# Kernel optimization log

Measured on AMD Instinct MI355X. Metric: run time of the kernel, lower is better.

The kernel has to match this reference:

```python
import jax, jax.numpy as jnp
import numpy as np

LATENT = 256
OUT_CH = 1
K = 16
HEADS = 64


def _conv1x1(x, W, b):
    # x: [B, Cin, ...spatial], W: [Cout, Cin], b: [Cout]
    y = jnp.einsum('oc,bc...->bo...', W, x)
    return y + b.reshape((1, -1) + (1,) * (y.ndim - 2))


def _batch_gather(x, idx):
    # x: [B, C, N], idx: [B, Nq, K] -> [B, C, Nq, K]
    return jax.vmap(lambda xb, ib: xb[:, ib])(x, idx)


def setup_inputs() -> dict:
    key = jax.random.key(0)
    ks = jax.random.split(key, 16)
    B, N, NQ = 2, 10000, 10000
    inp = {
        'latents': jax.random.normal(ks[0], (B, LATENT, N), jnp.float32),
        'pts': jax.random.normal(ks[1], (B, 3, N), jnp.float32),
        'pts_query': jax.random.normal(ks[2], (B, 3, NQ), jnp.float32),
        'proj_ids': jax.random.randint(ks[3], (B, NQ, K), 0, N, jnp.int64),
    }
    def lin(k, o, i):
        s = 1.0 / np.sqrt(i)
        k1, k2 = jax.random.split(k)
        return (jax.random.uniform(k1, (o, i), jnp.float32, -s, s),
                jax.random.uniform(k2, (o,), jnp.float32, -s, s))
    inp['W1'], inp['b1'] = lin(ks[4], LATENT, LATENT + 3)
    inp['W2'], inp['b2'] = lin(ks[5], LATENT, LATENT)
    inp['W3'], inp['b3'] = lin(ks[6], LATENT, LATENT)
    inp['Wq'], inp['bq'] = lin(ks[7], HEADS, LATENT)
    inp['Wv'], inp['bv'] = lin(ks[8], LATENT, LATENT)
    inp['W8'], inp['b8'] = lin(ks[9], OUT_CH, LATENT)
    return inp


def reference(latents, pts, pts_query, proj_ids,
              W1, b1, W2, b2, W3, b3, Wq, bq, Wv, bv, W8, b8):
    # gather neighbor latents and points: [B, C, Nq, K], [B, 3, Nq, K]
    x = _batch_gather(latents, proj_ids)
    npts = _batch_gather(pts, proj_ids)
    rel = pts_query[:, :, :, None] - npts          # [B, 3, Nq, K]
    x = jnp.concatenate([x, rel], axis=1)          # [B, C+3, Nq, K]
    x = jax.nn.relu(_conv1x1(x, W1, b1))
    x = jax.nn.relu(_conv1x1(x, W2, b2))
    x = jax.nn.relu(_conv1x1(x, W3, b3))
    query = _conv1x1(x, Wq, bq)                    # [B, 64, Nq, K]
    value = _conv1x1(x, Wv, bv)                    # [B, C, Nq, K]
    attention = jax.nn.softmax(query, axis=-1).mean(axis=1)  # [B, Nq, K]
    # weighted sum over K neighbors: [B, Nq, C] -> [B, C, Nq]
    x = jnp.einsum('bnk,bcnk->bcn', attention, value)
    x = _conv1x1(x, W8, b8)                        # [B, out_ch, Nq]
    return x
```

## Files before the change

kernel.cpp:

```cpp
#include <hip/hip_runtime.h>
#include <cstdint>
#include <cstddef>


#define NLAT 256
#define KNB 16
#define QB 4
#define MROWS 64
#define ROWB 560

typedef float    f32x4  __attribute__((ext_vector_type(4)));
typedef float    f32x16 __attribute__((ext_vector_type(16)));
typedef _Float16 f16x8  __attribute__((ext_vector_type(8)));
typedef _Float16 f16x4  __attribute__((ext_vector_type(4)));

struct Smem {
  unsigned char buf[MROWS * ROWB];
  float Sp[4][MROWS];
  float Sv[MROWS];
  int sidx[MROWS];
  int is64;
};

__device__ __forceinline__ void layer_mfma32(
    unsigned char* __restrict__ buf, const unsigned short* __restrict__ Wp,
    const float* __restrict__ bias, const float* __restrict__ W1f,
    int lane, int wave, bool relu)
{
  const int lm32 = lane & 31, h = lane >> 5;
  const char* bp = (const char*)buf + lm32 * 560 + h * 16;
  const char* wbase = (const char*)Wp + (wave * 2) * 1024 + lm32 * 32 + h * 16;

  f32x16 acc[2][2];
#pragma unroll
  for (int i = 0; i < 2; ++i)
#pragma unroll
    for (int j = 0; j < 2; ++j) acc[i][j] = (f32x16)(0.f);

#pragma unroll
  for (int ks = 0; ks < 16; ++ks) {
    f16x8 a[2], b[2];
#pragma unroll
    for (int ct = 0; ct < 2; ++ct)
      a[ct] = *(const f16x8*)(wbase + ks * 8192 + ct * 1024);
#pragma unroll
    for (int mt = 0; mt < 2; ++mt)
      b[mt] = *(const f16x8*)(bp + mt * 17920 + ks * 32);
#pragma unroll
    for (int ct = 0; ct < 2; ++ct)
#pragma unroll
      for (int mt = 0; mt < 2; ++mt)
        acc[ct][mt] = __builtin_amdgcn_mfma_f32_32x32x16_f16(a[ct], b[mt], acc[ct][mt], 0, 0, 0);
  }
  if (W1f) {
    f16x8 a[2], b[2];
#pragma unroll
    for (int ct = 0; ct < 2; ++ct) {
      f16x8 v = {0, 0, 0, 0, 0, 0, 0, 0};
      if (h == 0) {
        const int ch = (wave * 2 + ct) * 32 + lm32;
        const float* wt = W1f + (size_t)ch * 259 + 256;
        v[0] = (_Float16)wt[0]; v[1] = (_Float16)wt[1]; v[2] = (_Float16)wt[2];
      }
      a[ct] = v;
    }
#pragma unroll
    for (int mt = 0; mt < 2; ++mt)
      b[mt] = *(const f16x8*)(bp + mt * 17920 + 512);
#pragma unroll
    for (int ct = 0; ct < 2; ++ct)
#pragma unroll
      for (int mt = 0; mt < 2; ++mt)
        acc[ct][mt] = __builtin_amdgcn_mfma_f32_32x32x16_f16(a[ct], b[mt], acc[ct][mt], 0, 0, 0);
  }
  __syncthreads();
#pragma unroll
  for (int ct = 0; ct < 2; ++ct) {
#pragma unroll
    for (int q = 0; q < 4; ++q) {
      const int ch0 = (wave * 2 + ct) * 32 + q * 8 + h * 4;
      const float4 bs = *(const float4*)(bias + ch0);
      const float bb[4] = {bs.x, bs.y, bs.z, bs.w};
#pragma unroll
      for (int mt = 0; mt < 2; ++mt) {
        f16x4 v;
#pragma unroll
        for (int j = 0; j < 4; ++j) {
          float x = acc[ct][mt][q * 4 + j] + bb[j];
          if (relu) x = fmaxf(x, 0.f);
          v[j] = (_Float16)x;
        }
        *(f16x4*)((char*)buf + (mt * 32 + lm32) * 560 + ch0 * 2) = v;
      }
    }
  }
}

extern "C" __global__ __launch_bounds__(256, 4)
void interp_mfma(const float* __restrict__ latents,
                 const float* __restrict__ pts,
                 const float* __restrict__ ptsq,
                 const void*  __restrict__ proj,
                 const unsigned short* __restrict__ Lt_u,
                 const float* __restrict__ W1f,
                 const unsigned short* __restrict__ W1p,
                 const unsigned short* __restrict__ W2p,
                 const unsigned short* __restrict__ W3p,
                 const unsigned short* __restrict__ Wqh,
                 const float* __restrict__ b1, const float* __restrict__ b2,
                 const float* __restrict__ b3, const float* __restrict__ bq,
                 const float* __restrict__ wv8, const float* __restrict__ c0p,
                 float* __restrict__ out,
                 int N, int NQ, int use_lt)
{
  __shared__ Smem sm;
  const int tid = threadIdx.x;
  const int bid = blockIdx.x;
  const int lane = tid & 63, wave = tid >> 6;
  const int lm = lane & 15, lk = lane >> 4;

  if (tid == 0) {
    const int* p = (const int*)proj;
    int z = 1;
    for (int i = 0; i < 64; ++i) z &= (p[2 * i + 1] == 0);
    sm.is64 = z;
  }
  __syncthreads();
  if (tid < MROWS) {
    long long g = (long long)bid * QB + (tid >> 4);
    long long base = g * KNB + (tid & 15);
    sm.sidx[tid] = sm.is64 ? (int)((const long long*)proj)[base]
                           : ((const int*)proj)[base];
  }
  __syncthreads();

  {
    const int row = tid & 63, part = tid >> 6;
    const int id = sm.sidx[row];
    const long long g = (long long)bid * QB + (row >> 4);
    const int b = (int)(g / NQ);
    char* dst = (char*)sm.buf + row * 560 + part * 128;
    if (use_lt) {
      const _Float16* src = (const _Float16*)Lt_u + ((size_t)b * N + id) * NLAT + part * 64;
#pragma unroll
      for (int cc = 0; cc < 8; ++cc)
        *(f16x8*)(dst + cc * 16) = *(const f16x8*)(src + cc * 8);
    } else {
      for (int cc = 0; cc < 8; ++cc) {
        f16x8 v;
#pragma unroll
        for (int e = 0; e < 8; ++e)
          v[e] = (_Float16)latents[((size_t)b * NLAT + part * 64 + cc * 8 + e) * N + id];
        *(f16x8*)(dst + cc * 16) = v;
      }
    }
    if (part == 0) {
      const int nq = (int)(g - (long long)b * NQ);
      f16x8 v = {0, 0, 0, 0, 0, 0, 0, 0};
#pragma unroll
      for (int j = 0; j < 3; ++j)
        v[j] = (_Float16)(ptsq[((size_t)b * 3 + j) * NQ + nq]
                        - pts[((size_t)b * 3 + j) * N + id]);
      const f16x8 z = {0, 0, 0, 0, 0, 0, 0, 0};
      *(f16x8*)((char*)sm.buf + row * 560 + 512) = v;
      *(f16x8*)((char*)sm.buf + row * 560 + 528) = z;
    }
  }
  __syncthreads();

  layer_mfma32(sm.buf, W1p, b1, W1f, lane, wave, true);
  __syncthreads();
  layer_mfma32(sm.buf, W2p, b2, nullptr, lane, wave, true);
  __syncthreads();
  layer_mfma32(sm.buf, W3p, b3, nullptr, lane, wave, true);
  __syncthreads();

  const char* bp16 = (const char*)sm.buf + lm * 560 + lk * 16;
  f32x4 qacc[4];
#pragma unroll
  for (int mt = 0; mt < 4; ++mt) qacc[mt] = (f32x4){0.f, 0.f, 0.f, 0.f};
  {
    const char* wqb = (const char*)Wqh + (wave * 16 + lm) * 512 + lk * 16;
#pragma unroll
    for (int ks = 0; ks < 8; ++ks) {
      f16x8 a = *(const f16x8*)(wqb + ks * 64);
#pragma unroll
      for (int mt = 0; mt < 4; ++mt) {
        f16x8 bf = *(const f16x8*)(bp16 + mt * 8960 + ks * 64);
        qacc[mt] = __builtin_amdgcn_mfma_f32_16x16x32_f16(a, bf, qacc[mt], 0, 0, 0);
      }
    }
  }
  {
    const char* sp = (const char*)sm.buf + (wave * 16 + lm) * 560 + lk * 16;
    float sacc = 0.f;
#pragma unroll
    for (int cc = 0; cc < 8; ++cc) {
      f16x8 v = *(const f16x8*)(sp + cc * 64);
      const int k0 = cc * 32 + lk * 8;
      const float4 w0 = *(const float4*)(wv8 + k0);
      const float4 w1 = *(const float4*)(wv8 + k0 + 4);
      sacc += (float)v[0] * w0.x + (float)v[1] * w0.y
            + (float)v[2] * w0.z + (float)v[3] * w0.w;
      sacc += (float)v[4] * w1.x + (float)v[5] * w1.y
            + (float)v[6] * w1.z + (float)v[7] * w1.w;
    }
    sacc += __shfl_xor(sacc, 16);
    sacc += __shfl_xor(sacc, 32);
    if (lk == 0) sm.Sv[wave * 16 + lm] = sacc;
  }

  {
    float bqv[4];
#pragma unroll
    for (int r = 0; r < 4; ++r) bqv[r] = bq[wave * 16 + lk * 4 + r];
#pragma unroll
    for (int mt = 0; mt < 4; ++mt) {
      float sw = 0.f;
#pragma unroll
      for (int r = 0; r < 4; ++r) {
        const float qv = qacc[mt][r] + bqv[r];
        float mx = qv;
#pragma unroll
        for (int msk = 1; msk < 16; msk <<= 1) mx = fmaxf(mx, __shfl_xor(mx, msk));
        const float e = __expf(qv - mx);
        float s = e;
#pragma unroll
        for (int msk = 1; msk < 16; msk <<= 1) s += __shfl_xor(s, msk);
        sw += e / s;
      }
      sw += __shfl_xor(sw, 16);
      sw += __shfl_xor(sw, 32);
      if (lk == 0) sm.Sp[wave][mt * 16 + lm] = sw;
    }
  }
  __syncthreads();

  {
    const int m = wave * 16 + lm;
    const float a = (sm.Sp[0][m] + sm.Sp[1][m] + sm.Sp[2][m] + sm.Sp[3][m]) * (1.f / 64.f);
    float val = a * sm.Sv[m];
#pragma unroll
    for (int msk = 1; msk < 16; msk <<= 1) val += __shfl_xor(val, msk);
    if (lane == 0) out[(long long)bid * QB + wave] = val + c0p[0];
  }
}

extern "C" __global__ void prep_w(const float* __restrict__ W1, const float* __restrict__ W2,
                                  const float* __restrict__ W3, const float* __restrict__ Wq,
                                  const float* __restrict__ Wv, const float* __restrict__ W8,
                                  const float* __restrict__ bv, const float* __restrict__ b8,
                                  unsigned short* W1p, unsigned short* W2p,
                                  unsigned short* W3p, unsigned short* Wqh,
                                  float* wv8, float* c0) {
  const int t = blockIdx.x * 256 + threadIdx.x;
  union { _Float16 h; unsigned short u; } cv;
  if (t < 65536) {
    const int ch = t >> 8, k = t & 255;
    const int dst = (k >> 4) * 4096 + ch * 16 + ((k >> 3) & 1) * 8 + (k & 7);
    cv.h = (_Float16)W1[(size_t)ch * 259 + k]; W1p[dst] = cv.u;
    cv.h = (_Float16)W2[t]; W2p[dst] = cv.u;
    cv.h = (_Float16)W3[t]; W3p[dst] = cv.u;
  }
  if (t < 16384) { cv.h = (_Float16)Wq[t]; Wqh[t] = cv.u; }
  if (t < 256) {
    float s = 0.f;
    for (int o = 0; o < 256; ++o) s += Wv[(size_t)o * 256 + t] * W8[o];
    wv8[t] = s;
  }
  if (t == 0) {
    float s = 0.f;
    for (int o = 0; o < 256; ++o) s += bv[o] * W8[o];
    c0[0] = s + b8[0];
  }
}

extern "C" __global__ void transp(const float* __restrict__ latents,
                                  unsigned short* __restrict__ Lt, int N) {
  __shared__ unsigned short tile[256][68];
  const int b = blockIdx.y, n0 = blockIdx.x * 64, tid = threadIdx.x;
  const int nl = tid & 63;
  union { _Float16 h; unsigned short u; } cv;
  for (int c = tid >> 6; c < 256; c += 4) {
    const int n = n0 + nl;
    float v = (n < N) ? latents[((size_t)b * NLAT + c) * N + n] : 0.f;
    cv.h = (_Float16)v;
    tile[c][nl] = cv.u;
  }
  __syncthreads();
  const int nr = tid >> 2, cg = (tid & 3) * 64;
  const int n = n0 + nr;
  if (n < N) {
    for (int cc = 0; cc < 64; cc += 8) {
      f16x8 v;
#pragma unroll
      for (int j = 0; j < 8; ++j) {
        union { unsigned short u; _Float16 h; } bk;
        bk.u = tile[cg + cc + j][nr];
        v[j] = bk.h;
      }
      *(f16x8*)((_Float16*)Lt + ((size_t)b * N + n) * NLAT + cg + cc) = v;
    }
  }
}

extern "C" void kernel_launch(void* const* d_in, const int* in_sizes, int n_in,
                              void* d_out, int out_size, void* d_ws, size_t ws_size,
                              hipStream_t stream) {
  (void)n_in; (void)out_size;
  const float* latents = (const float*)d_in[0];
  const float* pts     = (const float*)d_in[1];
  const float* ptsq    = (const float*)d_in[2];
  const void*  proj    = d_in[3];
  const float* W1 = (const float*)d_in[4];  const float* b1 = (const float*)d_in[5];
  const float* W2 = (const float*)d_in[6];  const float* b2 = (const float*)d_in[7];
  const float* W3 = (const float*)d_in[8];  const float* b3 = (const float*)d_in[9];
  const float* Wq = (const float*)d_in[10]; const float* bq = (const float*)d_in[11];
  const float* Wv = (const float*)d_in[12]; const float* bv = (const float*)d_in[13];
  const float* W8 = (const float*)d_in[14]; const float* b8 = (const float*)d_in[15];
  float* out = (float*)d_out;

  const int B  = 2;
  const int N  = in_sizes[1] / (3 * B);
  const int NQ = in_sizes[2] / (3 * B);

  size_t off = 0;
  auto alloc = [&](size_t bytes) -> char* {
    char* p = (char*)d_ws + off;
    off += (bytes + 255) & ~(size_t)255;
    return p;
  };
  unsigned short* W1p = (unsigned short*)alloc(65536 * 2);
  unsigned short* W2p = (unsigned short*)alloc(65536 * 2);
  unsigned short* W3p = (unsigned short*)alloc(65536 * 2);
  unsigned short* Wqh = (unsigned short*)alloc(16384 * 2);
  float* wv8 = (float*)alloc(256 * 4);
  float* c0  = (float*)alloc(4);
  const size_t lt_bytes = (size_t)B * N * NLAT * 2;
  unsigned short* Lt = (unsigned short*)((char*)d_ws + off);
  const int use_lt = (off + lt_bytes <= ws_size) ? 1 : 0;

  hipLaunchKernelGGL(prep_w, dim3(256), dim3(256), 0, stream,
                     W1, W2, W3, Wq, Wv, W8, bv, b8, W1p, W2p, W3p, Wqh, wv8, c0);
  if (use_lt)
    hipLaunchKernelGGL(transp, dim3((N + 63) / 64, B), dim3(256), 0, stream,
                       latents, Lt, N);
  const int nblocks = (B * NQ + QB - 1) / QB;
  hipLaunchKernelGGL(interp_mfma, dim3(nblocks), dim3(256), 0, stream,
                     latents, pts, ptsq, proj, Lt, W1, W1p, W2p, W3p, Wqh,
                     b1, b2, b3, bq, wv8, c0, out, N, NQ, use_lt);
}
```

Measured before the change: 219.5 us.

## Double rows per block and give each wave full query heads locally

```diff
diff --git a/kernel.cpp b/kernel.cpp
--- a/kernel.cpp
+++ b/kernel.cpp
@@ -5,22 +5,14 @@
 
 #define NLAT 256
 #define KNB 16
-#define QB 4
-#define MROWS 64
+#define QB 8
+#define MROWS 128
 #define ROWB 560
 
 typedef float    f32x4  __attribute__((ext_vector_type(4)));
 typedef float    f32x16 __attribute__((ext_vector_type(16)));
 typedef _Float16 f16x8  __attribute__((ext_vector_type(8)));
 typedef _Float16 f16x4  __attribute__((ext_vector_type(4)));
-
-struct Smem {
-  unsigned char buf[MROWS * ROWB];
-  float Sp[4][MROWS];
-  float Sv[MROWS];
-  int sidx[MROWS];
-  int is64;
-};
 
 __device__ __forceinline__ void layer_mfma32(
     unsigned char* __restrict__ buf, const unsigned short* __restrict__ Wp,
@@ -29,48 +21,48 @@
 {
   const int lm32 = lane & 31, h = lane >> 5;
   const char* bp = (const char*)buf + lm32 * 560 + h * 16;
-  const char* wbase = (const char*)Wp + (wave * 2) * 1024 + lm32 * 32 + h * 16;
-
-  f32x16 acc[2][2];
+  const char* wbase = (const char*)Wp + (wave * 64 + lm32) * 32 + h * 16;
+
+  f32x16 acc[2][4];
 #pragma unroll
   for (int i = 0; i < 2; ++i)
 #pragma unroll
-    for (int j = 0; j < 2; ++j) acc[i][j] = (f32x16)(0.f);
+    for (int j = 0; j < 4; ++j) acc[i][j] = (f32x16)(0.f);
 
 #pragma unroll
   for (int ks = 0; ks < 16; ++ks) {
-    f16x8 a[2], b[2];
+    f16x8 a[2], b[4];
 #pragma unroll
     for (int ct = 0; ct < 2; ++ct)
       a[ct] = *(const f16x8*)(wbase + ks * 8192 + ct * 1024);
 #pragma unroll
-    for (int mt = 0; mt < 2; ++mt)
+    for (int mt = 0; mt < 4; ++mt)
       b[mt] = *(const f16x8*)(bp + mt * 17920 + ks * 32);
 #pragma unroll
     for (int ct = 0; ct < 2; ++ct)
 #pragma unroll
-      for (int mt = 0; mt < 2; ++mt)
+      for (int mt = 0; mt < 4; ++mt)
         acc[ct][mt] = __builtin_amdgcn_mfma_f32_32x32x16_f16(a[ct], b[mt], acc[ct][mt], 0, 0, 0);
   }
   if (W1f) {
-    f16x8 a[2], b[2];
+    f16x8 a[2], b[4];
 #pragma unroll
     for (int ct = 0; ct < 2; ++ct) {
       f16x8 v = {0, 0, 0, 0, 0, 0, 0, 0};
       if (h == 0) {
-        const int ch = (wave * 2 + ct) * 32 + lm32;
+        const int ch = wave * 64 + ct * 32 + lm32;
         const float* wt = W1f + (size_t)ch * 259 + 256;
         v[0] = (_Float16)wt[0]; v[1] = (_Float16)wt[1]; v[2] = (_Float16)wt[2];
       }
       a[ct] = v;
     }
 #pragma unroll
-    for (int mt = 0; mt < 2; ++mt)
+    for (int mt = 0; mt < 4; ++mt)
       b[mt] = *(const f16x8*)(bp + mt * 17920 + 512);
 #pragma unroll
     for (int ct = 0; ct < 2; ++ct)
 #pragma unroll
-      for (int mt = 0; mt < 2; ++mt)
+      for (int mt = 0; mt < 4; ++mt)
         acc[ct][mt] = __builtin_amdgcn_mfma_f32_32x32x16_f16(a[ct], b[mt], acc[ct][mt], 0, 0, 0);
   }
   __syncthreads();
@@ -78,11 +70,11 @@
   for (int ct = 0; ct < 2; ++ct) {
 #pragma unroll
     for (int q = 0; q < 4; ++q) {
-      const int ch0 = (wave * 2 + ct) * 32 + q * 8 + h * 4;
+      const int ch0 = wave * 64 + ct * 32 + q * 8 + h * 4;
       const float4 bs = *(const float4*)(bias + ch0);
       const float bb[4] = {bs.x, bs.y, bs.z, bs.w};
 #pragma unroll
-      for (int mt = 0; mt < 2; ++mt) {
+      for (int mt = 0; mt < 4; ++mt) {
         f16x4 v;
 #pragma unroll
         for (int j = 0; j < 4; ++j) {
@@ -96,7 +88,7 @@
   }
 }
 
-extern "C" __global__ __launch_bounds__(256, 4)
+extern "C" __global__ __launch_bounds__(256, 2)
 void interp_mfma(const float* __restrict__ latents,
                  const float* __restrict__ pts,
                  const float* __restrict__ ptsq,
@@ -113,44 +105,39 @@
                  float* __restrict__ out,
                  int N, int NQ, int use_lt)
 {
-  __shared__ Smem sm;
+  __shared__ unsigned char buf[MROWS * ROWB];
   const int tid = threadIdx.x;
   const int bid = blockIdx.x;
   const int lane = tid & 63, wave = tid >> 6;
   const int lm = lane & 15, lk = lane >> 4;
 
-  if (tid == 0) {
+  int is64;
+  {
     const int* p = (const int*)proj;
     int z = 1;
     for (int i = 0; i < 64; ++i) z &= (p[2 * i + 1] == 0);
-    sm.is64 = z;
-  }
-  __syncthreads();
-  if (tid < MROWS) {
-    long long g = (long long)bid * QB + (tid >> 4);
-    long long base = g * KNB + (tid & 15);
-    sm.sidx[tid] = sm.is64 ? (int)((const long long*)proj)[base]
-                           : ((const int*)proj)[base];
-  }
-  __syncthreads();
+    is64 = z;
+  }
 
   {
-    const int row = tid & 63, part = tid >> 6;
-    const int id = sm.sidx[row];
+    const int row = tid & 127, part = tid >> 7;
     const long long g = (long long)bid * QB + (row >> 4);
+    const long long pbase = g * KNB + (row & 15);
+    const int id = is64 ? (int)((const long long*)proj)[pbase]
+                        : ((const int*)proj)[pbase];
     const int b = (int)(g / NQ);
-    char* dst = (char*)sm.buf + row * 560 + part * 128;
+    char* dst = (char*)buf + row * 560 + part * 256;
     if (use_lt) {
-      const _Float16* src = (const _Float16*)Lt_u + ((size_t)b * N + id) * NLAT + part * 64;
-#pragma unroll
-      for (int cc = 0; cc < 8; ++cc)
+      const _Float16* src = (const _Float16*)Lt_u + ((size_t)b * N + id) * NLAT + part * 128;
+#pragma unroll
+      for (int cc = 0; cc < 16; ++cc)
         *(f16x8*)(dst + cc * 16) = *(const f16x8*)(src + cc * 8);
     } else {
-      for (int cc = 0; cc < 8; ++cc) {
+      for (int cc = 0; cc < 16; ++cc) {
         f16x8 v;
 #pragma unroll
         for (int e = 0; e < 8; ++e)
-          v[e] = (_Float16)latents[((size_t)b * NLAT + part * 64 + cc * 8 + e) * N + id];
+          v[e] = (_Float16)latents[((size_t)b * NLAT + part * 128 + cc * 8 + e) * N + id];
         *(f16x8*)(dst + cc * 16) = v;
       }
     }
@@ -162,37 +149,47 @@
         v[j] = (_Float16)(ptsq[((size_t)b * 3 + j) * NQ + nq]
                         - pts[((size_t)b * 3 + j) * N + id]);
       const f16x8 z = {0, 0, 0, 0, 0, 0, 0, 0};
-      *(f16x8*)((char*)sm.buf + row * 560 + 512) = v;
-      *(f16x8*)((char*)sm.buf + row * 560 + 528) = z;
-    }
-  }
-  __syncthreads();
-
-  layer_mfma32(sm.buf, W1p, b1, W1f, lane, wave, true);
-  __syncthreads();
-  layer_mfma32(sm.buf, W2p, b2, nullptr, lane, wave, true);
-  __syncthreads();
-  layer_mfma32(sm.buf, W3p, b3, nullptr, lane, wave, true);
-  __syncthreads();
-
-  const char* bp16 = (const char*)sm.buf + lm * 560 + lk * 16;
-  f32x4 qacc[4];
-#pragma unroll
-  for (int mt = 0; mt < 4; ++mt) qacc[mt] = (f32x4){0.f, 0.f, 0.f, 0.f};
+      *(f16x8*)((char*)buf + row * 560 + 512) = v;
+      *(f16x8*)((char*)buf + row * 560 + 528) = z;
+    }
+  }
+  __syncthreads();
+
+  layer_mfma32(buf, W1p, b1, W1f, lane, wave, true);
+  __syncthreads();
+  layer_mfma32(buf, W2p, b2, nullptr, lane, wave, true);
+  __syncthreads();
+  layer_mfma32(buf, W3p, b3, nullptr, lane, wave, true);
+  __syncthreads();
+
+  const char* bp16 = (const char*)buf + (wave * 32 + lm) * 560 + lk * 16;
+  f32x4 qacc[4][2];
+#pragma unroll
+  for (int ht = 0; ht < 4; ++ht)
+#pragma unroll
+    for (int mt = 0; mt < 2; ++mt) qacc[ht][mt] = (f32x4){0.f, 0.f, 0.f, 0.f};
   {
-    const char* wqb = (const char*)Wqh + (wave * 16 + lm) * 512 + lk * 16;
 #pragma unroll
     for (int ks = 0; ks < 8; ++ks) {
-      f16x8 a = *(const f16x8*)(wqb + ks * 64);
-#pragma unroll
-      for (int mt = 0; mt < 4; ++mt) {
-        f16x8 bf = *(const f16x8*)(bp16 + mt * 8960 + ks * 64);
-        qacc[mt] = __builtin_amdgcn_mfma_f32_16x16x32_f16(a, bf, qacc[mt], 0, 0, 0);
-      }
-    }
-  }
-  {
-    const char* sp = (const char*)sm.buf + (wave * 16 + lm) * 560 + lk * 16;
+      f16x8 a[4], b[2];
+#pragma unroll
+      for (int ht = 0; ht < 4; ++ht)
+        a[ht] = *(const f16x8*)((const char*)Wqh + (ht * 16 + lm) * 512 + ks * 64 + lk * 16);
+#pragma unroll
+      for (int mt = 0; mt < 2; ++mt)
+        b[mt] = *(const f16x8*)(bp16 + mt * 8960 + ks * 64);
+#pragma unroll
+      for (int ht = 0; ht < 4; ++ht)
+#pragma unroll
+        for (int mt = 0; mt < 2; ++mt)
+          qacc[ht][mt] = __builtin_amdgcn_mfma_f32_16x16x32_f16(a[ht], b[mt], qacc[ht][mt], 0, 0, 0);
+    }
+  }
+
+  float sv[2];
+#pragma unroll
+  for (int sg = 0; sg < 2; ++sg) {
+    const char* sp = (const char*)buf + (wave * 32 + sg * 16 + lm) * 560 + lk * 16;
     float sacc = 0.f;
 #pragma unroll
     for (int cc = 0; cc < 8; ++cc) {
@@ -207,42 +204,41 @@
     }
     sacc += __shfl_xor(sacc, 16);
     sacc += __shfl_xor(sacc, 32);
-    if (lk == 0) sm.Sv[wave * 16 + lm] = sacc;
+    sv[sg] = sacc;
   }
 
   {
-    float bqv[4];
-#pragma unroll
-    for (int r = 0; r < 4; ++r) bqv[r] = bq[wave * 16 + lk * 4 + r];
-#pragma unroll
-    for (int mt = 0; mt < 4; ++mt) {
+    float bqv[4][4];
+#pragma unroll
+    for (int ht = 0; ht < 4; ++ht) {
+      const float4 bv4 = *(const float4*)(bq + ht * 16 + lk * 4);
+      bqv[ht][0] = bv4.x; bqv[ht][1] = bv4.y; bqv[ht][2] = bv4.z; bqv[ht][3] = bv4.w;
+    }
+#pragma unroll
+    for (int sg = 0; sg < 2; ++sg) {
       float sw = 0.f;
 #pragma unroll
-      for (int r = 0; r < 4; ++r) {
-        const float qv = qacc[mt][r] + bqv[r];
-        float mx = qv;
-#pragma unroll
-        for (int msk = 1; msk < 16; msk <<= 1) mx = fmaxf(mx, __shfl_xor(mx, msk));
-        const float e = __expf(qv - mx);
-        float s = e;
-#pragma unroll
-        for (int msk = 1; msk < 16; msk <<= 1) s += __shfl_xor(s, msk);
-        sw += e / s;
+      for (int ht = 0; ht < 4; ++ht) {
+#pragma unroll
+        for (int r = 0; r < 4; ++r) {
+          const float qv = qacc[ht][sg][r] + bqv[ht][r];
+          float mx = qv;
+#pragma unroll
+          for (int msk = 1; msk < 16; msk <<= 1) mx = fmaxf(mx, __shfl_xor(mx, msk));
+          const float e = __expf(qv - mx);
+          float s = e;
+#pragma unroll
+          for (int msk = 1; msk < 16; msk <<= 1) s += __shfl_xor(s, msk);
+          sw += e / s;
+        }
       }
       sw += __shfl_xor(sw, 16);
       sw += __shfl_xor(sw, 32);
-      if (lk == 0) sm.Sp[wave][mt * 16 + lm] = sw;
-    }
-  }
-  __syncthreads();
-
-  {
-    const int m = wave * 16 + lm;
-    const float a = (sm.Sp[0][m] + sm.Sp[1][m] + sm.Sp[2][m] + sm.Sp[3][m]) * (1.f / 64.f);
-    float val = a * sm.Sv[m];
-#pragma unroll
-    for (int msk = 1; msk < 16; msk <<= 1) val += __shfl_xor(val, msk);
-    if (lane == 0) out[(long long)bid * QB + wave] = val + c0p[0];
+      float val = sw * (1.f / 64.f) * sv[sg];
+#pragma unroll
+      for (int msk = 1; msk < 16; msk <<= 1) val += __shfl_xor(val, msk);
+      if (lane == 0) out[(long long)bid * QB + wave * 2 + sg] = val + c0p[0];
+    }
   }
 }
 
```

Result: slower. 248.8 us (+13.4%).

## Precompute layer-1 projection per source point before gathering neighbors

Applied to the files above, without the earlier changes.

```diff
diff --git a/kernel.cpp b/kernel.cpp
--- a/kernel.cpp
+++ b/kernel.cpp
@@ -7,7 +7,8 @@
 #define KNB 16
 #define QB 4
 #define MROWS 64
-#define ROWB 560
+#define ROWB 528
+#define MTSTR 16896
 
 typedef float    f32x4  __attribute__((ext_vector_type(4)));
 typedef float    f32x16 __attribute__((ext_vector_type(16)));
@@ -24,12 +25,11 @@
 
 __device__ __forceinline__ void layer_mfma32(
     unsigned char* __restrict__ buf, const unsigned short* __restrict__ Wp,
-    const float* __restrict__ bias, const float* __restrict__ W1f,
-    int lane, int wave, bool relu)
+    const float* __restrict__ bias, int lane, int wave, bool relu)
 {
   const int lm32 = lane & 31, h = lane >> 5;
-  const char* bp = (const char*)buf + lm32 * 560 + h * 16;
-  const char* wbase = (const char*)Wp + (wave * 2) * 1024 + lm32 * 32 + h * 16;
+  const char* bp = (const char*)buf + lm32 * 528 + h * 16;
+  const char* wbase = (const char*)Wp + (wave * 64 + lm32) * 32 + h * 16;
 
   f32x16 acc[2][2];
 #pragma unroll
@@ -45,40 +45,19 @@
       a[ct] = *(const f16x8*)(wbase + ks * 8192 + ct * 1024);
 #pragma unroll
     for (int mt = 0; mt < 2; ++mt)
-      b[mt] = *(const f16x8*)(bp + mt * 17920 + ks * 32);
+      b[mt] = *(const f16x8*)(bp + mt * MTSTR + ks * 32);
 #pragma unroll
     for (int ct = 0; ct < 2; ++ct)
 #pragma unroll
       for (int mt = 0; mt < 2; ++mt)
         acc[ct][mt] = __builtin_amdgcn_mfma_f32_32x32x16_f16(a[ct], b[mt], acc[ct][mt], 0, 0, 0);
   }
-  if (W1f) {
-    f16x8 a[2], b[2];
-#pragma unroll
-    for (int ct = 0; ct < 2; ++ct) {
-      f16x8 v = {0, 0, 0, 0, 0, 0, 0, 0};
-      if (h == 0) {
-        const int ch = (wave * 2 + ct) * 32 + lm32;
-        const float* wt = W1f + (size_t)ch * 259 + 256;
-        v[0] = (_Float16)wt[0]; v[1] = (_Float16)wt[1]; v[2] = (_Float16)wt[2];
-      }
-      a[ct] = v;
-    }
-#pragma unroll
-    for (int mt = 0; mt < 2; ++mt)
-      b[mt] = *(const f16x8*)(bp + mt * 17920 + 512);
-#pragma unroll
-    for (int ct = 0; ct < 2; ++ct)
-#pragma unroll
-      for (int mt = 0; mt < 2; ++mt)
-        acc[ct][mt] = __builtin_amdgcn_mfma_f32_32x32x16_f16(a[ct], b[mt], acc[ct][mt], 0, 0, 0);
-  }
   __syncthreads();
 #pragma unroll
   for (int ct = 0; ct < 2; ++ct) {
 #pragma unroll
     for (int q = 0; q < 4; ++q) {
-      const int ch0 = (wave * 2 + ct) * 32 + q * 8 + h * 4;
+      const int ch0 = wave * 64 + ct * 32 + q * 8 + h * 4;
       const float4 bs = *(const float4*)(bias + ch0);
       const float bb[4] = {bs.x, bs.y, bs.z, bs.w};
 #pragma unroll
@@ -90,28 +69,26 @@
           if (relu) x = fmaxf(x, 0.f);
           v[j] = (_Float16)x;
         }
-        *(f16x4*)((char*)buf + (mt * 32 + lm32) * 560 + ch0 * 2) = v;
+        *(f16x4*)((char*)buf + (mt * 32 + lm32) * 528 + ch0 * 2) = v;
       }
     }
   }
 }
 
 extern "C" __global__ __launch_bounds__(256, 4)
-void interp_mfma(const float* __restrict__ latents,
-                 const float* __restrict__ pts,
+void interp_mfma(const float* __restrict__ pts,
                  const float* __restrict__ ptsq,
                  const void*  __restrict__ proj,
-                 const unsigned short* __restrict__ Lt_u,
-                 const float* __restrict__ W1f,
-                 const unsigned short* __restrict__ W1p,
+                 const unsigned short* __restrict__ L1pre,
+                 const float* __restrict__ w1rT,
                  const unsigned short* __restrict__ W2p,
                  const unsigned short* __restrict__ W3p,
                  const unsigned short* __restrict__ Wqh,
-                 const float* __restrict__ b1, const float* __restrict__ b2,
-                 const float* __restrict__ b3, const float* __restrict__ bq,
+                 const float* __restrict__ b2, const float* __restrict__ b3,
+                 const float* __restrict__ bq,
                  const float* __restrict__ wv8, const float* __restrict__ c0p,
                  float* __restrict__ out,
-                 int N, int NQ, int use_lt)
+                 int N, int NQ)
 {
   __shared__ Smem sm;
   const int tid = threadIdx.x;
@@ -139,43 +116,43 @@
     const int id = sm.sidx[row];
     const long long g = (long long)bid * QB + (row >> 4);
     const int b = (int)(g / NQ);
-    char* dst = (char*)sm.buf + row * 560 + part * 128;
-    if (use_lt) {
-      const _Float16* src = (const _Float16*)Lt_u + ((size_t)b * N + id) * NLAT + part * 64;
-#pragma unroll
-      for (int cc = 0; cc < 8; ++cc)
-        *(f16x8*)(dst + cc * 16) = *(const f16x8*)(src + cc * 8);
-    } else {
-      for (int cc = 0; cc < 8; ++cc) {
-        f16x8 v;
-#pragma unroll
-        for (int e = 0; e < 8; ++e)
-          v[e] = (_Float16)latents[((size_t)b * NLAT + part * 64 + cc * 8 + e) * N + id];
-        *(f16x8*)(dst + cc * 16) = v;
-      }
-    }
-    if (part == 0) {
-      const int nq = (int)(g - (long long)b * NQ);
-      f16x8 v = {0, 0, 0, 0, 0, 0, 0, 0};
-#pragma unroll
-      for (int j = 0; j < 3; ++j)
-        v[j] = (_Float16)(ptsq[((size_t)b * 3 + j) * NQ + nq]
-                        - pts[((size_t)b * 3 + j) * N + id]);
-      const f16x8 z = {0, 0, 0, 0, 0, 0, 0, 0};
-      *(f16x8*)((char*)sm.buf + row * 560 + 512) = v;
-      *(f16x8*)((char*)sm.buf + row * 560 + 528) = z;
-    }
-  }
-  __syncthreads();
-
-  layer_mfma32(sm.buf, W1p, b1, W1f, lane, wave, true);
-  __syncthreads();
-  layer_mfma32(sm.buf, W2p, b2, nullptr, lane, wave, true);
-  __syncthreads();
-  layer_mfma32(sm.buf, W3p, b3, nullptr, lane, wave, true);
-  __syncthreads();
-
-  const char* bp16 = (const char*)sm.buf + lm * 560 + lk * 16;
+    const int nq = (int)(g - (long long)b * NQ);
+    float rel[3];
+#pragma unroll
+    for (int j = 0; j < 3; ++j)
+      rel[j] = ptsq[((size_t)b * 3 + j) * NQ + nq]
+             - pts[((size_t)b * 3 + j) * N + id];
+    const _Float16* lp = (const _Float16*)L1pre + ((size_t)b * N + id) * NLAT + part * 64;
+    const float* wr0 = w1rT + part * 64;
+    const float* wr1 = w1rT + 256 + part * 64;
+    const float* wr2 = w1rT + 512 + part * 64;
+    char* dst = (char*)sm.buf + row * 528 + part * 128;
+#pragma unroll
+    for (int cc = 0; cc < 8; ++cc) {
+      f16x8 v = *(const f16x8*)(lp + cc * 8);
+      const float4 a0 = *(const float4*)(wr0 + cc * 8), a1 = *(const float4*)(wr0 + cc * 8 + 4);
+      const float4 b0 = *(const float4*)(wr1 + cc * 8), b1_ = *(const float4*)(wr1 + cc * 8 + 4);
+      const float4 c0 = *(const float4*)(wr2 + cc * 8), c1 = *(const float4*)(wr2 + cc * 8 + 4);
+      const float wa[8] = {a0.x, a0.y, a0.z, a0.w, a1.x, a1.y, a1.z, a1.w};
+      const float wb[8] = {b0.x, b0.y, b0.z, b0.w, b1_.x, b1_.y, b1_.z, b1_.w};
+      const float wc[8] = {c0.x, c0.y, c0.z, c0.w, c1.x, c1.y, c1.z, c1.w};
+      f16x8 o;
+#pragma unroll
+      for (int e = 0; e < 8; ++e) {
+        float x = (float)v[e] + rel[0] * wa[e] + rel[1] * wb[e] + rel[2] * wc[e];
+        o[e] = (_Float16)fmaxf(x, 0.f);
+      }
+      *(f16x8*)(dst + cc * 16) = o;
+    }
+  }
+  __syncthreads();
+
+  layer_mfma32(sm.buf, W2p, b2, lane, wave, true);
+  __syncthreads();
+  layer_mfma32(sm.buf, W3p, b3, lane, wave, true);
+  __syncthreads();
+
+  const char* bp16 = (const char*)sm.buf + lm * 528 + lk * 16;
   f32x4 qacc[4];
 #pragma unroll
   for (int mt = 0; mt < 4; ++mt) qacc[mt] = (f32x4){0.f, 0.f, 0.f, 0.f};
@@ -186,13 +163,13 @@
       f16x8 a = *(const f16x8*)(wqb + ks * 64);
 #pragma unroll
       for (int mt = 0; mt < 4; ++mt) {
-        f16x8 bf = *(const f16x8*)(bp16 + mt * 8960 + ks * 64);
+        f16x8 bf = *(const f16x8*)(bp16 + mt * 8448 + ks * 64);
         qacc[mt] = __builtin_amdgcn_mfma_f32_16x16x32_f16(a, bf, qacc[mt], 0, 0, 0);
       }
     }
   }
   {
-    const char* sp = (const char*)sm.buf + (wave * 16 + lm) * 560 + lk * 16;
+    const char* sp = (const char*)sm.buf + (wave * 16 + lm) * 528 + lk * 16;
     float sacc = 0.f;
 #pragma unroll
     for (int cc = 0; cc < 8; ++cc) {
@@ -246,23 +223,111 @@
   }
 }
 
+extern "C" __global__ __launch_bounds__(256, 4)
+void l1pre_k(const unsigned short* __restrict__ Lt_u,
+             const float* __restrict__ latents,
+             const unsigned short* __restrict__ W1p,
+             const float* __restrict__ b1,
+             unsigned short* __restrict__ L1pre, int N, int use_lt)
+{
+  __shared__ unsigned char buf[MROWS * ROWB];
+  const int tid = threadIdx.x;
+  const int b = blockIdx.y, n0 = blockIdx.x * 64;
+  const int lane = tid & 63, wave = tid >> 6;
+  const int lm32 = lane & 31, h = lane >> 5;
+
+  {
+    const int row = tid & 63, part = tid >> 6;
+    const int n = n0 + row;
+    char* dst = (char*)buf + row * 528 + part * 128;
+    if (n < N) {
+      if (use_lt) {
+        const _Float16* src = (const _Float16*)Lt_u + ((size_t)b * N + n) * NLAT + part * 64;
+#pragma unroll
+        for (int cc = 0; cc < 8; ++cc)
+          *(f16x8*)(dst + cc * 16) = *(const f16x8*)(src + cc * 8);
+      } else {
+        for (int cc = 0; cc < 8; ++cc) {
+          f16x8 v;
+#pragma unroll
+          for (int e = 0; e < 8; ++e)
+            v[e] = (_Float16)latents[((size_t)b * NLAT + part * 64 + cc * 8 + e) * N + n];
+          *(f16x8*)(dst + cc * 16) = v;
+        }
+      }
+    } else {
+      const f16x8 z = {0, 0, 0, 0, 0, 0, 0, 0};
+#pragma unroll
+      for (int cc = 0; cc < 8; ++cc) *(f16x8*)(dst + cc * 16) = z;
+    }
+  }
+  __syncthreads();
+
+  const char* bp = (const char*)buf + lm32 * 528 + h * 16;
+  const char* wbase = (const char*)W1p + (wave * 64 + lm32) * 32 + h * 16;
+  f32x16 acc[2][2];
+#pragma unroll
+  for (int i = 0; i < 2; ++i)
+#pragma unroll
+    for (int j = 0; j < 2; ++j) acc[i][j] = (f32x16)(0.f);
+#pragma unroll
+  for (int ks = 0; ks < 16; ++ks) {
+    f16x8 a[2], bb[2];
+#pragma unroll
+    for (int ct = 0; ct < 2; ++ct)
+      a[ct] = *(const f16x8*)(wbase + ks * 8192 + ct * 1024);
+#pragma unroll
+    for (int mt = 0; mt < 2; ++mt)
+      bb[mt] = *(const f16x8*)(bp + mt * MTSTR + ks * 32);
+#pragma unroll
+    for (int ct = 0; ct < 2; ++ct)
+#pragma unroll
+      for (int mt = 0; mt < 2; ++mt)
+        acc[ct][mt] = __builtin_amdgcn_mfma_f32_32x32x16_f16(a[ct], bb[mt], acc[ct][mt], 0, 0, 0);
+  }
+#pragma unroll
+  for (int ct = 0; ct < 2; ++ct) {
+#pragma unroll
+    for (int q = 0; q < 4; ++q) {
+      const int ch0 = wave * 64 + ct * 32 + q * 8 + h * 4;
+      const float4 bs = *(const float4*)(b1 + ch0);
+      const float bb[4] = {bs.x, bs.y, bs.z, bs.w};
+#pragma unroll
+      for (int mt = 0; mt < 2; ++mt) {
+        const int n = n0 + mt * 32 + lm32;
+        if (n < N) {
+          f16x4 v;
+#pragma unroll
+          for (int j = 0; j < 4; ++j)
+            v[j] = (_Float16)(acc[ct][mt][q * 4 + j] + bb[j]);
+          *(f16x4*)((char*)L1pre + (((size_t)b * N + n) * NLAT + ch0) * 2) = v;
+        }
+      }
+    }
+  }
+}
+
 extern "C" __global__ void prep_w(const float* __restrict__ W1, const float* __restrict__ W2,
                                   const float* __restrict__ W3, const float* __restrict__ Wq,
                                   const float* __restrict__ Wv, const float* __restrict__ W8,
                                   const float* __restrict__ bv, const float* __restrict__ b8,
                                   unsigned short* W1p, unsigned short* W2p,
                                   unsigned short* W3p, unsigned short* Wqh,
-                                  float* wv8, float* c0) {
+                                  float* w1rT, float* wv8, float* c0) {
   const int t = blockIdx.x * 256 + threadIdx.x;
   union { _Float16 h; unsigned short u; } cv;
   if (t < 65536) {
     const int ch = t >> 8, k = t & 255;
-    const int dst = (k >> 4) * 4096 + ch * 16 + ((k >> 3) & 1) * 8 + (k & 7);
+    const int dst = (k >> 4) * 4096 + ch * 16 + (k & 15);
     cv.h = (_Float16)W1[(size_t)ch * 259 + k]; W1p[dst] = cv.u;
     cv.h = (_Float16)W2[t]; W2p[dst] = cv.u;
     cv.h = (_Float16)W3[t]; W3p[dst] = cv.u;
   }
   if (t < 16384) { cv.h = (_Float16)Wq[t]; Wqh[t] = cv.u; }
+  if (t < 768) {
+    const int j = t >> 8, ch = t & 255;
+    w1rT[t] = W1[(size_t)ch * 259 + 256 + j];
+  }
   if (t < 256) {
     float s = 0.f;
     for (int o = 0; o < 256; ++o) s += Wv[(size_t)o * 256 + t] * W8[o];
@@ -334,19 +399,24 @@
   unsigned short* W2p = (unsigned short*)alloc(65536 * 2);
   unsigned short* W3p = (unsigned short*)alloc(65536 * 2);
   unsigned short* Wqh = (unsigned short*)alloc(16384 * 2);
-  float* wv8 = (float*)alloc(256 * 4);
-  float* c0  = (float*)alloc(4);
-  const size_t lt_bytes = (size_t)B * N * NLAT * 2;
+  float* w1rT = (float*)alloc(768 * 4);
+  float* wv8  = (float*)alloc(256 * 4);
+  float* c0   = (float*)alloc(4);
+  const size_t l1_bytes = (size_t)B * N * NLAT * 2;
+  unsigned short* L1pre = (unsigned short*)alloc(l1_bytes);
   unsigned short* Lt = (unsigned short*)((char*)d_ws + off);
-  const int use_lt = (off + lt_bytes <= ws_size) ? 1 : 0;
+  const int use_lt = (off + l1_bytes <= ws_size) ? 1 : 0;
 
   hipLaunchKernelGGL(prep_w, dim3(256), dim3(256), 0, stream,
-                     W1, W2, W3, Wq, Wv, W8, bv, b8, W1p, W2p, W3p, Wqh, wv8, c0);
+                     W1, W2, W3, Wq, Wv, W8, bv, b8, W1p, W2p, W3p, Wqh,
+                     w1rT, wv8, c0);
   if (use_lt)
     hipLaunchKernelGGL(transp, dim3((N + 63) / 64, B), dim3(256), 0, stream,
                        latents, Lt, N);
+  hipLaunchKernelGGL(l1pre_k, dim3((N + 63) / 64, B), dim3(256), 0, stream,
+                     Lt, latents, W1p, b1, L1pre, N, use_lt);
   const int nblocks = (B * NQ + QB - 1) / QB;
   hipLaunchKernelGGL(interp_mfma, dim3(nblocks), dim3(256), 0, stream,
-                     latents, pts, ptsq, proj, Lt, W1, W1p, W2p, W3p, Wqh,
-                     b1, b2, b3, bq, wv8, c0, out, N, NQ, use_lt);
-}
+                     pts, ptsq, proj, L1pre, w1rT, W2p, W3p, Wqh,
+                     b2, b3, bq, wv8, c0, out, N, NQ);
+}
```

Result: faster. 210.4 us (-4.1%).
